# Optimization experiments

Hardware: AMD Instinct MI355X
Metric: run time of the kernel (lower is better)

## Reference

```python
import jax, jax.numpy as jnp
import numpy as np


def setup_inputs() -> dict:
    key = jax.random.key(0)
    k1, k2 = jax.random.split(key)
    N, D = 8192, 256
    cond_feature = jax.random.normal(k1, (N, D), dtype=jnp.float32)
    sol_feature = jax.random.normal(k2, (N, D), dtype=jnp.float32)
    temperature = jnp.asarray(0.5, dtype=jnp.float32)  # learned scalar, used as exp(temperature)
    return {"cond_feature": cond_feature, "sol_feature": sol_feature, "temperature": temperature}


def reference(cond_feature, sol_feature, temperature):
    N = cond_feature.shape[0]
    c = cond_feature.reshape(N, -1)  # [N, D]
    s = sol_feature.reshape(sol_feature.shape[0], -1)  # [N, D]
    # pairwise L2 distance via ||a||^2 + ||b||^2 - 2 a.b (avoids N x N x D intermediate)
    c2 = jnp.sum(c * c, axis=-1)  # [N]
    s2 = jnp.sum(s * s, axis=-1)  # [N]
    d2 = c2[:, None] + s2[None, :] - 2.0 * jnp.einsum('nd,md->nm', c, s)
    dist = jnp.sqrt(jnp.maximum(d2, 0.0))  # [N, N]
    sim = -dist * jnp.exp(temperature)
    # cross_entropy(sim, arange) + cross_entropy(sim.T, arange): diagonal of log-softmax both ways
    logp_row = jax.nn.log_softmax(sim, axis=-1)  # CE over rows
    logp_col = jax.nn.log_softmax(sim, axis=0)   # CE over columns == CE(sim.T, labels)
    diag = jnp.arange(N)
    loss_row = -jnp.mean(logp_row[diag, diag])
    loss_col = -jnp.mean(logp_col[diag, diag])
    return (loss_row + loss_col) * 0.5
```

## Files before the change

kernel.cpp:

```cpp
#include <hip/hip_runtime.h>
#include <math.h>

#define DIM 256
#define TM 256
#define TN 128
#define BK 64

typedef __bf16 bf16x8 __attribute__((ext_vector_type(8)));
typedef float f32x4 __attribute__((ext_vector_type(4)));

typedef const __attribute__((address_space(1))) void* gas_ptr;
typedef __attribute__((address_space(3))) void* las_ptr;

__device__ __forceinline__ void async_cp16(const void* g, void* l) {
    __builtin_amdgcn_global_load_lds((gas_ptr)g, (las_ptr)l, 16, 0, 0);
}

__device__ __forceinline__ unsigned short f32_to_bf16(float f) {
    unsigned int u = __float_as_uint(f);
    u += 0x7FFFu + ((u >> 16) & 1u);
    return (unsigned short)(u >> 16);
}

__global__ __launch_bounds__(256) void convert_kernel(
        const float* __restrict__ C, const float* __restrict__ S,
        unsigned short* __restrict__ Cb, unsigned short* __restrict__ Sb,
        float* __restrict__ c2, float* __restrict__ s2,
        float* __restrict__ ddot, float* __restrict__ sums0,
        float* __restrict__ out, int N) {
    int gtid = blockIdx.x * 256 + threadIdx.x;
    if (gtid < 2 * N) sums0[gtid] = 0.0f;
    if (gtid == 0) out[0] = 0.0f;
    int row = gtid >> 6;
    int lane = gtid & 63;
    if (row >= N) return;
    float4 v  = ((const float4*)(C + (size_t)row * DIM))[lane];
    float4 sv = ((const float4*)(S + (size_t)row * DIM))[lane];
    ushort4 bc, bs;
    bc.x = f32_to_bf16(v.x);  bc.y = f32_to_bf16(v.y);
    bc.z = f32_to_bf16(v.z);  bc.w = f32_to_bf16(v.w);
    bs.x = f32_to_bf16(sv.x); bs.y = f32_to_bf16(sv.y);
    bs.z = f32_to_bf16(sv.z); bs.w = f32_to_bf16(sv.w);
    ((ushort4*)(Cb + (size_t)row * DIM))[lane] = bc;
    ((ushort4*)(Sb + (size_t)row * DIM))[lane] = bs;
    float nc = v.x * v.x + v.y * v.y + v.z * v.z + v.w * v.w;
    float ns = sv.x * sv.x + sv.y * sv.y + sv.z * sv.z + sv.w * sv.w;
    float cr = v.x * sv.x + v.y * sv.y + v.z * sv.z + v.w * sv.w;
    #pragma unroll
    for (int off = 32; off > 0; off >>= 1) {
        nc += __shfl_down(nc, off, 64);
        ns += __shfl_down(ns, off, 64);
        cr += __shfl_down(cr, off, 64);
    }
    if (lane == 0) { c2[row] = nc; s2[row] = ns; ddot[row] = cr; }
}

__global__ __launch_bounds__(512, 4) void mfma_kernel(
        const unsigned short* __restrict__ Cb, const unsigned short* __restrict__ Sb,
        const float* __restrict__ c2, const float* __restrict__ s2,
        const float* __restrict__ temp,
        float* __restrict__ rowsum, float* __restrict__ colsum, int N) {
    __shared__ __align__(16) unsigned short Abuf[TM * BK];
    __shared__ __align__(16) unsigned short Bbuf[TN * BK];
    __shared__ float rs[TM], cs[TN], c2t[TM], s2t[TN];

    const int tid = threadIdx.x;
    const int bm = blockIdx.y * TM;
    const int bn = blockIdx.x * TN;
    const int w  = tid >> 6;
    const int l  = tid & 63;
    const int wm = (w >> 1) * 64;
    const int wn = (w & 1) * 64;

    if (tid < TM) { rs[tid] = 0.0f; c2t[tid] = c2[bm + tid]; }
    else if (tid < TM + TN) {
        int t = tid - TM; cs[t] = 0.0f; s2t[t] = s2[bn + t];
    }

    const int l8 = l >> 3;
    const int gch = (l & 7) ^ l8;
    const unsigned short* gAl = Cb + (size_t)(bm + w * 8 + l8) * DIM + gch * 8;
    const unsigned short* gBl = Sb + (size_t)(bn + w * 8 + l8) * DIM + gch * 8;
    unsigned short* lA = &Abuf[w * 512];
    unsigned short* lB = &Bbuf[w * 512];
    const size_t istep = (size_t)64 * DIM;

    const int m16 = l & 15;
    const int q = l >> 4;
    const int m7 = m16 & 7;
    int aoff[4], boff[4];
    #pragma unroll
    for (int i = 0; i < 4; ++i) {
        aoff[i] = (wm + i * 16 + m16) * BK + ((q ^ m7) * 8);
        boff[i] = (wn + i * 16 + m16) * BK + ((q ^ m7) * 8);
    }

    f32x4 acc[4][4] = {};

    #pragma unroll
    for (int kk = 0; kk < 4; ++kk) {
        #pragma unroll
        for (int i = 0; i < 4; ++i) async_cp16(gAl + i * istep, lA + i * 4096);
        #pragma unroll
        for (int i = 0; i < 2; ++i) async_cp16(gBl + i * istep, lB + i * 4096);
        gAl += BK; gBl += BK;
        __syncthreads();

        #pragma unroll
        for (int t = 0; t < 2; ++t) {
            bf16x8 af[4], bf[4];
            #pragma unroll
            for (int i = 0; i < 4; ++i) af[i] = *(const bf16x8*)&Abuf[aoff[i] ^ (t << 5)];
            #pragma unroll
            for (int j = 0; j < 4; ++j) bf[j] = *(const bf16x8*)&Bbuf[boff[j] ^ (t << 5)];
            #pragma unroll
            for (int mi = 0; mi < 4; ++mi)
                #pragma unroll
                for (int ni = 0; ni < 4; ++ni)
                    acc[mi][ni] = __builtin_amdgcn_mfma_f32_16x16x32_bf16(
                        af[mi], bf[ni], acc[mi][ni], 0, 0, 0);
        }
        __syncthreads();
    }

    const float escale = __expf(temp[0]);

    float c2v[4][4], s2v[4];
    #pragma unroll
    for (int mi = 0; mi < 4; ++mi)
        #pragma unroll
        for (int r = 0; r < 4; ++r) c2v[mi][r] = c2t[wm + mi * 16 + q * 4 + r];
    #pragma unroll
    for (int ni = 0; ni < 4; ++ni) s2v[ni] = s2t[wn + ni * 16 + m16];

    float rp[16];
    #pragma unroll
    for (int s = 0; s < 16; ++s) rp[s] = 0.0f;
    float cp[4] = {0.f, 0.f, 0.f, 0.f};

    #pragma unroll
    for (int mi = 0; mi < 4; ++mi) {
        #pragma unroll
        for (int ni = 0; ni < 4; ++ni) {
            #pragma unroll
            for (int r = 0; r < 4; ++r) {
                float d2 = fmaf(-2.0f, acc[mi][ni][r], c2v[mi][r] + s2v[ni]);
                d2 = fmaxf(d2, 0.0f);
                float dist = __builtin_amdgcn_sqrtf(d2);
                float e = __expf(-escale * dist);
                rp[mi * 4 + r] += e;
                cp[ni] += e;
            }
        }
    }

    #pragma unroll
    for (int b = 0; b < 4; ++b) {
        const int n = 16 >> b;
        const int bit = (m16 >> b) & 1;
        #pragma unroll
        for (int k = 0; k < 8; ++k) {
            if (k < (n >> 1)) {
                float keep = bit ? rp[2 * k + 1] : rp[2 * k];
                float send = bit ? rp[2 * k] : rp[2 * k + 1];
                float recv = __shfl_xor(send, 1 << b, 64);
                rp[k] = keep + recv;
            }
        }
    }
    const int myrow = wm + (m16 >> 2) * 16 + q * 4 + (m16 & 3);
    atomicAdd(&rs[myrow], rp[0]);

    #pragma unroll
    for (int b = 0; b < 2; ++b) {
        const int n = 4 >> b;
        const int bit = (q >> b) & 1;
        #pragma unroll
        for (int k = 0; k < 2; ++k) {
            if (k < (n >> 1)) {
                float keep = bit ? cp[2 * k + 1] : cp[2 * k];
                float send = bit ? cp[2 * k] : cp[2 * k + 1];
                float recv = __shfl_xor(send, 16 << b, 64);
                cp[k] = keep + recv;
            }
        }
    }
    const int mycol = wn + q * 16 + m16;
    atomicAdd(&cs[mycol], cp[0]);

    __syncthreads();
    if (tid < TM) atomicAdd(&rowsum[bm + tid], rs[tid]);
    else if (tid < TM + TN) atomicAdd(&colsum[bn + tid - TM], cs[tid - TM]);
}

__global__ __launch_bounds__(256) void finalize_kernel(
        const float* __restrict__ rowsum, const float* __restrict__ colsum,
        const float* __restrict__ c2, const float* __restrict__ s2,
        const float* __restrict__ ddot, const float* __restrict__ temp,
        float* __restrict__ out, int N) {
    __shared__ float red[4];
    const float escale = __expf(temp[0]);
    const int tid = threadIdx.x;
    int i = blockIdx.x * 256 + tid;
    float sum = 0.0f;
    if (i < N) {
        float d2 = c2[i] + s2[i] - 2.0f * ddot[i];
        float dist = __builtin_amdgcn_sqrtf(fmaxf(d2, 0.0f));
        sum = __logf(rowsum[i]) + __logf(colsum[i]) + 2.0f * escale * dist;
    }
    #pragma unroll
    for (int off = 32; off > 0; off >>= 1) sum += __shfl_down(sum, off, 64);
    if ((tid & 63) == 0) red[tid >> 6] = sum;
    __syncthreads();
    if (tid == 0)
        atomicAdd(out, (red[0] + red[1] + red[2] + red[3]) / (2.0f * (float)N));
}

extern "C" void kernel_launch(void* const* d_in, const int* in_sizes, int n_in,
                              void* d_out, int out_size, void* d_ws, size_t ws_size,
                              hipStream_t stream) {
    const float* C = (const float*)d_in[0];
    const float* S = (const float*)d_in[1];
    const float* T = (const float*)d_in[2];
    const int N = in_sizes[0] / DIM;

    float* ws     = (float*)d_ws;
    float* c2     = ws;
    float* s2     = ws + N;
    float* rowsum = ws + 2 * N;
    float* colsum = ws + 3 * N;
    float* ddot   = ws + 4 * N;
    unsigned short* Cb = (unsigned short*)(ws + 5 * N + 64);
    unsigned short* Sb = Cb + (size_t)N * DIM;

    convert_kernel<<<(N * 64) / 256, 256, 0, stream>>>(
        C, S, Cb, Sb, c2, s2, ddot, rowsum, (float*)d_out, N);

    dim3 grid(N / TN, N / TM);
    mfma_kernel<<<grid, 512, 0, stream>>>(
        Cb, Sb, c2, s2, T, rowsum, colsum, N);

    finalize_kernel<<<(N + 255) / 256, 256, 0, stream>>>(
        rowsum, colsum, c2, s2, ddot, T, (float*)d_out, N);
}
```

Measured before the change: 122.4 us.

## Quantize operands to FP8 and use FP8 MFMA with permuted layout

Converts both feature matrices to FP8 (e4m3) instead of bf16, stored with a permuted byte layout so each lane can load 16 bytes holding two MFMA k-chunks. The GEMM uses the fp8 16x16x32 MFMA, which halves global and LDS traffic and the load instructions per k-step. It also folds exp(temperature)*log2(e) into the squared norms and the dot-product scale, so the epilogue is one sqrt plus exp2. FP8 cuts the precision of the dot products, and the loss may drift beyond tolerance because distances come from a cancelling subtraction.

Result: faster. 112.5 us (-8.1%).

```diff
diff --git a/kernel.cpp b/kernel.cpp
--- a/kernel.cpp
+++ b/kernel.cpp
@@ -6,8 +6,8 @@
 #define TN 128
 #define BK 64
 
-typedef __bf16 bf16x8 __attribute__((ext_vector_type(8)));
 typedef float f32x4 __attribute__((ext_vector_type(4)));
+typedef long long2v __attribute__((ext_vector_type(2)));
 
 typedef const __attribute__((address_space(1))) void* gas_ptr;
 typedef __attribute__((address_space(3))) void* las_ptr;
@@ -16,15 +16,9 @@
     __builtin_amdgcn_global_load_lds((gas_ptr)g, (las_ptr)l, 16, 0, 0);
 }
 
-__device__ __forceinline__ unsigned short f32_to_bf16(float f) {
-    unsigned int u = __float_as_uint(f);
-    u += 0x7FFFu + ((u >> 16) & 1u);
-    return (unsigned short)(u >> 16);
-}
-
 __global__ __launch_bounds__(256) void convert_kernel(
         const float* __restrict__ C, const float* __restrict__ S,
-        unsigned short* __restrict__ Cb, unsigned short* __restrict__ Sb,
+        unsigned char* __restrict__ Cb, unsigned char* __restrict__ Sb,
         float* __restrict__ c2, float* __restrict__ s2,
         float* __restrict__ ddot, float* __restrict__ sums0,
         float* __restrict__ out, int N) {
@@ -32,17 +26,17 @@
     if (gtid < 2 * N) sums0[gtid] = 0.0f;
     if (gtid == 0) out[0] = 0.0f;
     int row = gtid >> 6;
-    int lane = gtid & 63;
+    int l = gtid & 63;
     if (row >= N) return;
-    float4 v  = ((const float4*)(C + (size_t)row * DIM))[lane];
-    float4 sv = ((const float4*)(S + (size_t)row * DIM))[lane];
-    ushort4 bc, bs;
-    bc.x = f32_to_bf16(v.x);  bc.y = f32_to_bf16(v.y);
-    bc.z = f32_to_bf16(v.z);  bc.w = f32_to_bf16(v.w);
-    bs.x = f32_to_bf16(sv.x); bs.y = f32_to_bf16(sv.y);
-    bs.z = f32_to_bf16(sv.z); bs.w = f32_to_bf16(sv.w);
-    ((ushort4*)(Cb + (size_t)row * DIM))[lane] = bc;
-    ((ushort4*)(Sb + (size_t)row * DIM))[lane] = bs;
+    float4 v  = ((const float4*)(C + (size_t)row * DIM))[l];
+    float4 sv = ((const float4*)(S + (size_t)row * DIM))[l];
+    int pc = __builtin_amdgcn_cvt_pk_fp8_f32(v.x, v.y, 0, false);
+    pc     = __builtin_amdgcn_cvt_pk_fp8_f32(v.z, v.w, pc, true);
+    int ps = __builtin_amdgcn_cvt_pk_fp8_f32(sv.x, sv.y, 0, false);
+    ps     = __builtin_amdgcn_cvt_pk_fp8_f32(sv.z, sv.w, ps, true);
+    int idx4 = (l >> 4) * 16 + ((l & 7) >> 1) * 4 + ((l & 15) >> 3) * 2 + (l & 1);
+    ((int*)(Cb + (size_t)row * DIM))[idx4] = pc;
+    ((int*)(Sb + (size_t)row * DIM))[idx4] = ps;
     float nc = v.x * v.x + v.y * v.y + v.z * v.z + v.w * v.w;
     float ns = sv.x * sv.x + sv.y * sv.y + sv.z * sv.z + sv.w * sv.w;
     float cr = v.x * sv.x + v.y * sv.y + v.z * sv.z + v.w * sv.w;
@@ -52,16 +46,16 @@
         ns += __shfl_down(ns, off, 64);
         cr += __shfl_down(cr, off, 64);
     }
-    if (lane == 0) { c2[row] = nc; s2[row] = ns; ddot[row] = cr; }
+    if (l == 0) { c2[row] = nc; s2[row] = ns; ddot[row] = cr; }
 }
 
 __global__ __launch_bounds__(512, 4) void mfma_kernel(
-        const unsigned short* __restrict__ Cb, const unsigned short* __restrict__ Sb,
+        const unsigned char* __restrict__ Cb, const unsigned char* __restrict__ Sb,
         const float* __restrict__ c2, const float* __restrict__ s2,
         const float* __restrict__ temp,
         float* __restrict__ rowsum, float* __restrict__ colsum, int N) {
-    __shared__ __align__(16) unsigned short Abuf[TM * BK];
-    __shared__ __align__(16) unsigned short Bbuf[TN * BK];
+    __shared__ __align__(16) unsigned char Abuf[TM * BK];
+    __shared__ __align__(16) unsigned char Bbuf[TN * BK];
     __shared__ float rs[TM], cs[TN], c2t[TM], s2t[TN];
 
     const int tid = threadIdx.x;
@@ -72,58 +66,59 @@
     const int wm = (w >> 1) * 64;
     const int wn = (w & 1) * 64;
 
-    if (tid < TM) { rs[tid] = 0.0f; c2t[tid] = c2[bm + tid]; }
+    const float escale = __expf(temp[0]);
+    const float Kf = escale * 1.4426950408889634f;
+    const float K2 = Kf * Kf;
+    const float m2K2 = -2.0f * K2;
+
+    if (tid < TM) { rs[tid] = 0.0f; c2t[tid] = K2 * c2[bm + tid]; }
     else if (tid < TM + TN) {
-        int t = tid - TM; cs[t] = 0.0f; s2t[t] = s2[bn + t];
-    }
-
-    const int l8 = l >> 3;
-    const int gch = (l & 7) ^ l8;
-    const unsigned short* gAl = Cb + (size_t)(bm + w * 8 + l8) * DIM + gch * 8;
-    const unsigned short* gBl = Sb + (size_t)(bn + w * 8 + l8) * DIM + gch * 8;
-    unsigned short* lA = &Abuf[w * 512];
-    unsigned short* lB = &Bbuf[w * 512];
-    const size_t istep = (size_t)64 * DIM;
+        int t = tid - TM; cs[t] = 0.0f; s2t[t] = K2 * s2[bn + t];
+    }
+
+    const int l4 = l >> 2;
+    const int sc = (l & 3) ^ (l4 & 3);
+    const unsigned char* gA = Cb + (size_t)(bm + w * 16 + l4) * DIM + sc * 16;
+    const unsigned char* gB = Sb + (size_t)(bn + w * 16 + l4) * DIM + sc * 16;
+    unsigned char* lA = &Abuf[w * 1024];
+    unsigned char* lB = &Bbuf[w * 1024];
+    const size_t askip = (size_t)128 * DIM;
 
     const int m16 = l & 15;
     const int q = l >> 4;
-    const int m7 = m16 & 7;
     int aoff[4], boff[4];
     #pragma unroll
     for (int i = 0; i < 4; ++i) {
-        aoff[i] = (wm + i * 16 + m16) * BK + ((q ^ m7) * 8);
-        boff[i] = (wn + i * 16 + m16) * BK + ((q ^ m7) * 8);
+        aoff[i] = (wm + i * 16 + m16) * BK + ((q ^ (m16 & 3)) * 16);
+        boff[i] = (wn + i * 16 + m16) * BK + ((q ^ (m16 & 3)) * 16);
     }
 
     f32x4 acc[4][4] = {};
 
     #pragma unroll
     for (int kk = 0; kk < 4; ++kk) {
-        #pragma unroll
-        for (int i = 0; i < 4; ++i) async_cp16(gAl + i * istep, lA + i * 4096);
-        #pragma unroll
-        for (int i = 0; i < 2; ++i) async_cp16(gBl + i * istep, lB + i * 4096);
-        gAl += BK; gBl += BK;
+        async_cp16(gA, lA);
+        async_cp16(gA + askip, lA + 8192);
+        async_cp16(gB, lB);
+        gA += BK; gB += BK;
         __syncthreads();
 
-        #pragma unroll
-        for (int t = 0; t < 2; ++t) {
-            bf16x8 af[4], bf[4];
+        long2v af[4], bf[4];
+        #pragma unroll
+        for (int i = 0; i < 4; ++i) af[i] = *(const long2v*)&Abuf[aoff[i]];
+        #pragma unroll
+        for (int j = 0; j < 4; ++j) bf[j] = *(const long2v*)&Bbuf[boff[j]];
+        #pragma unroll
+        for (int mi = 0; mi < 4; ++mi)
             #pragma unroll
-            for (int i = 0; i < 4; ++i) af[i] = *(const bf16x8*)&Abuf[aoff[i] ^ (t << 5)];
-            #pragma unroll
-            for (int j = 0; j < 4; ++j) bf[j] = *(const bf16x8*)&Bbuf[boff[j] ^ (t << 5)];
-            #pragma unroll
-            for (int mi = 0; mi < 4; ++mi)
-                #pragma unroll
-                for (int ni = 0; ni < 4; ++ni)
-                    acc[mi][ni] = __builtin_amdgcn_mfma_f32_16x16x32_bf16(
-                        af[mi], bf[ni], acc[mi][ni], 0, 0, 0);
-        }
+            for (int ni = 0; ni < 4; ++ni) {
+                acc[mi][ni] = __builtin_amdgcn_mfma_f32_16x16x32_fp8_fp8(
+                    af[mi].x, bf[ni].x, acc[mi][ni], 0, 0, 0);
+                acc[mi][ni] = __builtin_amdgcn_mfma_f32_16x16x32_fp8_fp8(
+                    af[mi].y, bf[ni].y, acc[mi][ni], 0, 0, 0);
+            }
         __syncthreads();
     }
-
-    const float escale = __expf(temp[0]);
 
     float c2v[4][4], s2v[4];
     #pragma unroll
@@ -144,10 +139,9 @@
         for (int ni = 0; ni < 4; ++ni) {
             #pragma unroll
             for (int r = 0; r < 4; ++r) {
-                float d2 = fmaf(-2.0f, acc[mi][ni][r], c2v[mi][r] + s2v[ni]);
+                float d2 = fmaf(m2K2, acc[mi][ni][r], c2v[mi][r] + s2v[ni]);
                 d2 = fmaxf(d2, 0.0f);
-                float dist = __builtin_amdgcn_sqrtf(d2);
-                float e = __expf(-escale * dist);
+                float e = __builtin_amdgcn_exp2f(-__builtin_amdgcn_sqrtf(d2));
                 rp[mi * 4 + r] += e;
                 cp[ni] += e;
             }
@@ -230,8 +224,8 @@
     float* rowsum = ws + 2 * N;
     float* colsum = ws + 3 * N;
     float* ddot   = ws + 4 * N;
-    unsigned short* Cb = (unsigned short*)(ws + 5 * N + 64);
-    unsigned short* Sb = Cb + (size_t)N * DIM;
+    unsigned char* Cb = (unsigned char*)(ws + 5 * N + 64);
+    unsigned char* Sb = Cb + (size_t)N * DIM;
 
     convert_kernel<<<(N * 64) / 256, 256, 0, stream>>>(
         C, S, Cb, Sb, c2, s2, ddot, rowsum, (float*)d_out, N);
```
